# Optimization experiments

Measured on AMD Instinct MI355X. Metric: run time of the kernel, lower is better.

## Reference

```python
import jax, jax.numpy as jnp
import numpy as np

B_IN, B_L1, B_L2 = 64, 16, 8
F1, F2, F_OUT = 64, 128, 10
BATCH = 16
CPLX = jnp.complex64

# ---------- numpy precompute: quadrature weights, Wigner-d matrices, grids ----------

def _dh_weights(b):
    # Driscoll-Healy quadrature weights over the 2b beta samples
    j = np.arange(2 * b)
    l = np.arange(b)
    s = np.sin(np.outer(2 * j + 1, 2 * l + 1) * np.pi / (4 * b)) @ (1.0 / (2 * l + 1))
    return ((2.0 / b) * np.sin(np.pi * (2 * j + 1) / (4 * b)) * s).astype(np.float32)

def _wigner_d_all(lmax, betas):
    # d^l(beta) = exp(-i beta Jy) via eigendecomposition of Jy (quantum convention)
    betas = np.asarray(betas, np.float64)
    out = []
    for l in range(lmax + 1):
        m = np.arange(-l, l)
        cp = np.sqrt(l * (l + 1) - m * (m + 1))
        Jy = np.zeros((2 * l + 1, 2 * l + 1), np.complex128)
        Jy[np.arange(1, 2 * l + 1), np.arange(0, 2 * l)] = -0.5j * cp
        Jy[np.arange(0, 2 * l), np.arange(1, 2 * l + 1)] = 0.5j * cp
        lam, V = np.linalg.eigh(Jy)
        ph = np.exp(-1j * np.outer(betas, lam))
        d = np.einsum('mk,bk,nk->bmn', V, ph, V.conj())
        out.append(np.ascontiguousarray(d.real.astype(np.float32)))
    return out

def _s2_grid():
    beta = np.arange(1, 4) * (np.pi / 8) / 3
    alpha = np.linspace(0, 2 * np.pi, 8, endpoint=False)
    B, A = np.meshgrid(beta, alpha, indexing='ij')
    return B.ravel(), A.ravel()

def _so3_grid():
    beta = np.arange(1, 4) * (np.pi / 8) / 3
    alpha = np.linspace(0, 2 * np.pi, 8, endpoint=False)
    pre_gamma = np.linspace(0, 2 * np.pi, 8, endpoint=False)
    B, A, C = np.meshgrid(beta, alpha, pre_gamma, indexing='ij')
    return B.ravel(), A.ravel(), (C - A).ravel()

_BETAS_IN = np.pi * (2 * np.arange(2 * B_IN) + 1) / (4 * B_IN)
_BETAS_L1 = np.pi * (2 * np.arange(2 * B_L1) + 1) / (4 * B_L1)
_BETAS_L2 = np.pi * (2 * np.arange(2 * B_L2) + 1) / (4 * B_L2)
_W_IN = jnp.asarray(_dh_weights(B_IN))
_W_L1 = jnp.asarray(_dh_weights(B_L1))
_W_L2 = jnp.asarray(_dh_weights(B_L2))
_D_IN = _wigner_d_all(B_L1 - 1, _BETAS_IN)
_D_L1 = _wigner_d_all(B_L1 - 1, _BETAS_L1)
_D_L2 = _wigner_d_all(B_L2 - 1, _BETAS_L2)
_GB2, _GA2 = _s2_grid()
_GB3, _GA3, _GC3 = _so3_grid()
_D_G2 = _wigner_d_all(B_L1 - 1, _GB2)
_D_G3 = _wigner_d_all(B_L2 - 1, _GB3)

# spherical-harmonic / Wigner-D basis evaluated at kernel grid points
_PSI_S2 = []
for l in range(B_L1):
    m = np.arange(-l, l + 1)
    _PSI_S2.append(jnp.asarray((_D_G2[l][:, :, l].T * np.exp(-1j * np.outer(m, _GA2))).astype(np.complex64)))
_PSI_SO3 = []
for l in range(B_L2):
    m = np.arange(-l, l + 1)
    em = np.exp(-1j * np.outer(m, _GA3))
    en = np.exp(-1j * np.outer(m, _GC3))
    _PSI_SO3.append(jnp.asarray((_D_G3[l].transpose(1, 2, 0) * em[:, None, :] * en[None, :, :]).astype(np.complex64)))
_DCOL_IN = [jnp.asarray(_D_IN[l][:, :, l]) for l in range(B_L1)]  # d^l_{m,0}(beta_k)
_D_L1_J = [jnp.asarray(d) for d in _D_L1]
_D_L2_J = [jnp.asarray(d) for d in _D_L2]

# ---------- jax forward ----------

def _s2_fft(x):
    # x: [batch, f, 2b_in, 2b_in] (beta, alpha) -> list over l of [2l+1, batch, f] complex
    n = 2 * B_IN
    xf = jnp.fft.fft(x.astype(CPLX), axis=-1)  # e^{-i m alpha}
    out = []
    for l in range(B_L1):
        mi = np.arange(-l, l + 1) % n
        Xl = xf[..., mi]  # [batch, f, 2b, 2l+1]
        out.append(jnp.einsum('k,km,bfkm->mbf', _W_IN, _DCOL_IN[l], Xl) * (2 * np.pi / n))
    return out

def _so3_ifft(Fz, d_list, b):
    # Fz: list over l of [2l+1, 2l+1, batch, f] -> real [batch, f, 2b, 2b, 2b] (beta,alpha,gamma)
    n = 2 * b
    batch, f = Fz[0].shape[2], Fz[0].shape[3]
    S = jnp.zeros((batch, f, n, n, n), CPLX)
    for l in range(b):
        mi = np.arange(-l, l + 1) % n
        C = (2 * l + 1) * jnp.einsum('kmn,mnbf->bfkmn', d_list[l].astype(CPLX), Fz[l])
        S = S.at[:, :, :, mi[:, None], mi[None, :]].add(C)
    return jnp.real(jnp.fft.ifft2(S, axes=(-2, -1))) * (n * n)  # e^{+i m alpha} e^{+i n gamma}

def _so3_fft(x, d_list, w, b_l):
    # x: [batch, f, 2b, 2b, 2b] real -> list over l<b_l of [2l+1, 2l+1, batch, f] complex
    n = x.shape[-1]
    xf = jnp.fft.fft2(x.astype(CPLX), axes=(-2, -1)) / (n * n)
    out = []
    for l in range(b_l):
        mi = np.arange(-l, l + 1) % n
        Xl = xf[:, :, :, mi[:, None], mi[None, :]]  # [batch, f, 2b, 2l+1, 2l+1]
        out.append(jnp.einsum('k,kmn,bfkmn->mnbf', w, d_list[l], Xl) * (2 * np.pi))
    return out

def _forward(x, w1, w2, lin_w, lin_b):
    # S2Convolution: spectral x spectral-kernel outer product per degree l
    Fx = _s2_fft(x)
    Fy = [jnp.einsum('iog,mg->mio', w1.astype(CPLX), p) for p in _PSI_S2]
    Fz = [jnp.einsum('mbi,nio->mnbo', Fx[l], jnp.conj(Fy[l])) for l in range(B_L1)]
    y1 = jax.nn.relu(_so3_ifft(Fz, _D_L1_J, B_L1))
    # SO3Convolution
    Fx2 = _so3_fft(y1, _D_L1_J, _W_L1, B_L2)
    Fy2 = [jnp.einsum('iog,mng->mnio', w2.astype(CPLX), p) for p in _PSI_SO3]
    Fz2 = [jnp.einsum('mkbi,nkio->mnbo', Fx2[l], jnp.conj(Fy2[l])) for l in range(B_L2)]
    y2 = jax.nn.relu(_so3_ifft(Fz2, _D_L2_J, B_L2))
    # so3_integrate: quadrature over beta, uniform mean over alpha,gamma
    feat = jnp.einsum('k,bfk->bf', _W_L2, y2.mean(axis=(-2, -1)))
    return feat @ lin_w.T + lin_b


def setup_inputs() -> dict:
    key = jax.random.key(0)
    k1, k2, k3, k4 = jax.random.split(key, 4)
    x = jax.random.normal(k1, (BATCH, 1, 2 * B_IN, 2 * B_IN), jnp.float32)
    w1 = jax.random.normal(k2, (1, F1, 24), jnp.float32) / np.float32(np.sqrt(24))
    w2 = jax.random.normal(k3, (F1, F2, 192), jnp.float32) / np.float32(np.sqrt(192 * F1))
    lin_w = jax.random.normal(k4, (F_OUT, F2), jnp.float32) / np.float32(np.sqrt(F2))
    lin_b = jnp.zeros((F_OUT,), jnp.float32)
    return {'x': x, 'w1': w1, 'w2': w2, 'lin_w': lin_w, 'lin_b': lin_b}


def reference(x, w1, w2, lin_w, lin_b):
    return _forward(x, w1, w2, lin_w, lin_b)
```

## Files before the change

### kernel.cpp

```cpp
#include <hip/hip_runtime.h>
#include <cmath>
#include <vector>
#include <algorithm>

enum : int {
  OFF_WIN  = 0,
  OFF_WL1  = 128,
  OFF_WL2  = 160,
  OFF_DCOL = 176,
  OFF_D1A  = OFF_DCOL + 32768,
  OFF_D1B  = OFF_D1A + 174592,
  OFF_D2   = OFF_D1B + 174592,
  OFF_PSI2 = OFF_D2 + 10880,
  OFF_PSI3 = OFF_PSI2 + 12288,
  CONST_TOTAL = OFF_PSI3 + 261120
};

static constexpr size_t OFS_XF1  = 0;
static constexpr size_t OFS_FX   = 507904;
static constexpr size_t OFS_FY1  = 540672;
static constexpr size_t OFS_FX2  = 671744;
static constexpr size_t OFS_FY2  = 6242304;
static constexpr size_t OFS_FZ2  = 50806784;
static constexpr size_t OFS_W2T  = OFS_FZ2;
static constexpr size_t OFS_FEAT = 61947904;
static constexpr size_t WS_NEEDED = 61956096;

static inline int off3h(int l){ return (4*l*l*l - l)/3; }

namespace {

double fact_[32];
void init_fact(){ fact_[0]=1.0; for(int i=1;i<32;i++) fact_[i]=fact_[i-1]*i; }

void wigner_d(int l, double beta, double* d){
  int n = 2*l+1;
  double cb = std::cos(beta*0.5), sb = std::sin(beta*0.5);
  for(int r=0;r<n;r++){ int mp = r-l;
    for(int c=0;c<n;c++){ int m = c-l;
      double f = std::sqrt(fact_[l+mp]*fact_[l-mp]*fact_[l+m]*fact_[l-m]);
      int s0 = std::max(0, m-mp), s1 = std::min(l+m, l-mp);
      double sum = 0;
      for(int s=s0;s<=s1;s++){
        double t = (((mp-m+s)&1)? -1.0 : 1.0)
                 / (fact_[l+m-s]*fact_[s]*fact_[mp-m+s]*fact_[l-mp-s]);
        t *= std::pow(cb, (double)(2*l+m-mp-2*s)) * std::pow(sb, (double)(mp-m+2*s));
        sum += t;
      }
      d[r*n+c] = f*sum;
    }
  }
}

void dh_weights(int b, double* w){
  for(int j=0;j<2*b;j++){
    double s = 0;
    for(int l=0;l<b;l++) s += std::sin((2.0*j+1)*(2.0*l+1)*M_PI/(4.0*b))/(2.0*l+1);
    w[j] = (2.0/b)*std::sin(M_PI*(2.0*j+1)/(4.0*b))*s;
  }
}

float* g_const = nullptr;

struct ConstInit {
  ConstInit(){
    init_fact();
    std::vector<float> h((size_t)CONST_TOTAL, 0.0f);
    std::vector<double> tmp(31*31);
    std::vector<double> wl1(32);
    { std::vector<double> w(128); dh_weights(64, w.data()); for(int i=0;i<128;i++) h[OFF_WIN+i]=(float)w[i]; }
    { dh_weights(16, wl1.data()); for(int i=0;i<32;i++)  h[OFF_WL1+i]=(float)wl1[i]; }
    { std::vector<double> w(16);  dh_weights(8,  w.data()); for(int i=0;i<16;i++)  h[OFF_WL2+i]=(float)w[i]; }
    for(int l=0;l<16;l++){ int n=2*l+1;
      for(int k=0;k<128;k++){
        wigner_d(l, M_PI*(2.0*k+1)/256.0, tmp.data());
        for(int mi=0;mi<n;mi++) h[OFF_DCOL + (size_t)(l*l+mi)*128 + k] = (float)tmp[mi*n + l];
      }
    }
    for(int l=0;l<16;l++){ int n=2*l+1;
      for(int k=0;k<32;k++){
        wigner_d(l, M_PI*(2.0*k+1)/64.0, tmp.data());
        for(int t=0;t<n*n;t++){
          size_t base = (size_t)(off3h(l)+t)*32 + k;
          h[OFF_D1A + base] = (float)((2*l+1)*tmp[t]);
          if(l < 8)
            h[OFF_D1B + base] = (float)(2.0*M_PI*wl1[k]*tmp[t]/1024.0);
        }
      }
    }
    for(int l=0;l<8;l++){ int n=2*l+1;
      for(int k=0;k<16;k++){
        wigner_d(l, M_PI*(2.0*k+1)/32.0, tmp.data());
        for(int t=0;t<n*n;t++)
          h[OFF_D2 + (size_t)(off3h(l)+t)*16 + k] = (float)((2*l+1)*tmp[t]);
      }
    }
    for(int l=0;l<16;l++){ int n=2*l+1;
      for(int i=0;i<3;i++){
        wigner_d(l, (i+1)*(M_PI/8.0)/3.0, tmp.data());
        for(int j=0;j<8;j++){
          double alpha = 2.0*M_PI*j/8.0;
          int g = i*8+j;
          for(int mi=0;mi<n;mi++){
            double d = tmp[mi*n + l];
            double th = (double)(mi-l)*alpha;
            size_t base = OFF_PSI2 + ((size_t)(l*l+mi)*24 + g)*2;
            h[base+0] = (float)( d*std::cos(th));
            h[base+1] = (float)(-d*std::sin(th));
          }
        }
      }
    }
    for(int l=0;l<8;l++){ int n=2*l+1;
      for(int i=0;i<3;i++){
        wigner_d(l, (i+1)*(M_PI/8.0)/3.0, tmp.data());
        for(int j=0;j<8;j++){
          double alpha = 2.0*M_PI*j/8.0;
          for(int kk=0;kk<8;kk++){
            double gamma = 2.0*M_PI*kk/8.0 - alpha;
            int g = (i*8+j)*8+kk;
            for(int mi=0;mi<n;mi++) for(int ni=0;ni<n;ni++){
              double d = tmp[mi*n+ni];
              double th = (double)(mi-l)*alpha + (double)(ni-l)*gamma;
              size_t base = OFF_PSI3 + (((size_t)off3h(l)+ (size_t)mi*n+ni)*192 + g)*2;
              h[base+0] = (float)( d*std::cos(th));
              h[base+1] = (float)(-d*std::sin(th));
            }
          }
        }
      }
    }
    hipMalloc((void**)&g_const, sizeof(float)*(size_t)CONST_TOTAL);
    hipMemcpy(g_const, h.data(), sizeof(float)*(size_t)CONST_TOTAL, hipMemcpyHostToDevice);
  }
};
ConstInit g_init_;

}

__device__ __forceinline__ int off3d(int l){ return (4*l*l*l - l)/3; }
constexpr float TWO_PI_F = 6.28318530717958647692f;

__device__ __forceinline__ unsigned int f2bf(float f){
  union { float f; unsigned int u; } v; v.f = f;
  unsigned int r = v.u + 0x7FFFu + ((v.u >> 16) & 1u);
  return r >> 16;
}
__device__ __forceinline__ unsigned int pk2(float2 v){
  return f2bf(v.x) | (f2bf(v.y) << 16);
}
__device__ __forceinline__ float bflo(unsigned int u){
  union { unsigned int u; float f; } c; c.u = u << 16; return c.f;
}
__device__ __forceinline__ float bfhi(unsigned int u){
  union { unsigned int u; float f; } c; c.u = u & 0xffff0000u; return c.f;
}

typedef __attribute__((ext_vector_type(8))) short bf16x8;
typedef __attribute__((ext_vector_type(4))) float f32x4;

__global__ void k_fft_alpha(const float* __restrict__ x, float2* __restrict__ xf1){
  __shared__ float row[128];
  __shared__ float2 w128[128];
  __shared__ float2 red2[4][31];
  int r = blockIdx.x;
  int t = threadIdx.x;
  row[t] = x[(size_t)r*128 + t];
  float ang = (TWO_PI_F/128.0f)*t;
  w128[t] = make_float2(cosf(ang), sinf(ang));
  __syncthreads();
  int mi = t & 31, part = t >> 5;
  if(mi < 31){
    int m = mi - 15;
    float2 acc = make_float2(0.f,0.f);
    int a0 = part*32;
    for(int a=a0;a<a0+32;a++){
      float2 w = w128[(m*a)&127];
      acc.x += row[a]*w.x;
      acc.y -= row[a]*w.y;
    }
    red2[part][mi] = acc;
  }
  __syncthreads();
  if(t < 31){
    float2 s = red2[0][t];
    float2 s1 = red2[1][t], s2 = red2[2][t], s3 = red2[3][t];
    s.x += s1.x + s2.x + s3.x;
    s.y += s1.y + s2.y + s3.y;
    xf1[(size_t)r*31 + t] = s;
  }
}

__global__ void k_fx(const float* __restrict__ cst, const float2* __restrict__ xf1,
                     float2* __restrict__ FxP){
  __shared__ float2 redL[256];
  int lp = threadIdx.x & 63;
  int kc = threadIdx.x >> 6;
  int idx = blockIdx.x*64 + lp;
  int c2 = idx >> 4, b = idx & 15;
  int l = 0; while((l+1)*(l+1) <= c2) l++;
  int m = (c2 - l*l) - l;
  const float* W  = cst + OFF_WIN;
  const float* DC = cst + OFF_DCOL + (size_t)c2*128;
  float2 acc = make_float2(0.f,0.f);
  int k0 = kc*32;
  for(int k=k0;k<k0+32;k++){
    float wv = W[k]*DC[k];
    float2 xv = xf1[((size_t)b*128+k)*31 + (m+15)];
    acc.x += wv*xv.x; acc.y += wv*xv.y;
  }
  redL[threadIdx.x] = acc;
  __syncthreads();
  if(kc == 0){
    float2 p1 = redL[lp+64], p2 = redL[lp+128], p3 = redL[lp+192];
    acc.x += p1.x + p2.x + p3.x;
    acc.y += p1.y + p2.y + p3.y;
    float s = TWO_PI_F/128.0f;
    FxP[(size_t)c2*16+b] = make_float2(acc.x*s, acc.y*s);
  }
}

__global__ void k_fy1(const float* __restrict__ cst, const float* __restrict__ w1,
                      float2* __restrict__ FyP){
  int idx = blockIdx.x*blockDim.x + threadIdx.x;
  int c2 = idx >> 6, o = idx & 63;
  const float2* psi = (const float2*)(cst + OFF_PSI2) + (size_t)c2*24;
  const float* w1r = w1 + (size_t)o*24;
  float2 acc = make_float2(0.f,0.f);
  for(int g=0;g<24;g++){
    float wv = w1r[g];
    float2 p = psi[g];
    acc.x += wv*p.x; acc.y += wv*p.y;
  }
  FyP[(size_t)c2*64+o] = acc;
}

__global__ void __launch_bounds__(256,4) k_conv1(const float* __restrict__ cst,
                                                 const float2* __restrict__ FxP,
                                                 const float2* __restrict__ FyP,
                                                 unsigned int* __restrict__ FxB){
  __shared__ __align__(16) char L[39936];
  float2* FxL = (float2*)L;
  float2* FyL = FxL + 256;
  float2* SB  = (float2*)(L + 4096);
  unsigned int* yBu = (unsigned int*)(L + 4096);
  float2* XfB = (float2*)(L + 4096);
  unsigned int* TBu = (unsigned int*)(L + 23936);
  float2* T2B = (float2*)(L + 23936);
  float2* acc2= (float2*)(L + 34176);
  float2* w32 = (float2*)(L + 39616);
  int*    o3T = (int*)(L + 39872);

  int b = blockIdx.x >> 6, o = blockIdx.x & 63;
  int tid = threadIdx.x;
  if(tid < 32){ float ang = (TWO_PI_F/32.0f)*tid; w32[tid] = make_float2(cosf(ang), sinf(ang)); }
  if(tid < 16){ int l = tid; o3T[l] = (4*l*l*l - l)/3; }
  FxL[tid] = FxP[(size_t)tid*16 + b];
  FyL[tid] = FyP[(size_t)tid*64 + o];
  for(int t=tid; t<680; t+=256) acc2[t] = make_float2(0.f,0.f);

  const float* D1A = cst + OFF_D1A;
  const float* D1B = cst + OFF_D1B;

  for(int kt=0; kt<8; kt++){
    int k0 = kt*4;
    __syncthreads();
    for(int t=tid; t<496; t+=256){
      int mi = t/31, niq = t - mi*31;
      int n = niq-15;
      int an = n<0?-n:n;
      int lmin = mi>an?mi:an;
      float2 s0={0,0},s1={0,0},s2={0,0},s3={0,0};
      for(int l=lmin;l<16;l++){
        int c = 2*l+1, l2 = l*l;
        float2 fx = FxL[l2+l+mi];
        float2 fy = FyL[l2+(n+l)];
        float zx = fx.x*fy.x + fx.y*fy.y;
        float zy = fx.y*fy.x - fx.x*fy.y;
        const float4* dp = (const float4*)(D1A + (((size_t)o3T[l] + (mi+l)*c + (n+l))<<5) + k0);
        float4 d0 = dp[0];
        s0.x += d0.x*zx; s0.y += d0.x*zy;
        s1.x += d0.y*zx; s1.y += d0.y*zy;
        s2.x += d0.z*zx; s2.y += d0.z*zy;
        s3.x += d0.w*zx; s3.y += d0.w*zy;
      }
      float2* sp = SB + (size_t)t*5;
      sp[0]=s0; sp[1]=s1; sp[2]=s2; sp[3]=s3;
    }
    __syncthreads();
    {
      int mi = tid >> 4, cp = tid & 15;
      float2 a0[4], a1[4];
      #pragma unroll
      for(int j=0;j<4;j++){ a0[j]=make_float2(0,0); a1[j]=make_float2(0,0); }
      float2 step = w32[cp];
      float2 wv = w32[(15*cp)&31];
      float2 cur = make_float2(wv.x, -wv.y);
      const float2* srow = SB + (size_t)(mi*31)*5;
      for(int nb=0; nb<31; nb++){
        float2 q0 = srow[nb*5+0], q1 = srow[nb*5+1], q2 = srow[nb*5+2], q3 = srow[nb*5+3];
        float px, py;
        bool odd = (nb & 1);
        #define K1STEP(QX,QY,J) \
          px = QX*cur.x - QY*cur.y; py = QX*cur.y + QY*cur.x; \
          a0[J].x += px; a0[J].y += py; \
          if(odd){ a1[J].x += px; a1[J].y += py; } else { a1[J].x -= px; a1[J].y -= py; }
        K1STEP(q0.x,q0.y,0) K1STEP(q1.x,q1.y,1)
        K1STEP(q2.x,q2.y,2) K1STEP(q3.x,q3.y,3)
        #undef K1STEP
        float nx = cur.x*step.x - cur.y*step.y;
        cur.y = cur.x*step.y + cur.y*step.x;
        cur.x = nx;
      }
      unsigned int* tp0 = TBu + (size_t)(mi*32+cp)*5;
      tp0[0]=pk2(a0[0]); tp0[1]=pk2(a0[1]); tp0[2]=pk2(a0[2]); tp0[3]=pk2(a0[3]);
      unsigned int* tp1 = TBu + (size_t)(mi*32+cp+16)*5;
      tp1[0]=pk2(a1[0]); tp1[1]=pk2(a1[1]); tp1[2]=pk2(a1[2]); tp1[3]=pk2(a1[3]);
    }
    __syncthreads();
    {
      int c = tid & 31, aq = tid >> 5;
      float y0[4],y1[4],y2[4],y3[4], t0x[4];
      {
        const unsigned int* t0p = TBu + (size_t)c*5;
        t0x[0]=bflo(t0p[0]); t0x[1]=bflo(t0p[1]); t0x[2]=bflo(t0p[2]); t0x[3]=bflo(t0p[3]);
      }
      #pragma unroll
      for(int j=0;j<4;j++){ y0[j]=0; y1[j]=0; y2[j]=0; y3[j]=0; }
      #pragma unroll
      for(int m=1;m<16;m++){
        float2 w = w32[(m*aq)&31];
        const unsigned int* tp = TBu + (size_t)(m*32+c)*5;
        unsigned int d0=tp[0], d1=tp[1], d2=tp[2], d3=tp[3];
        float tx[4] = {bflo(d0),bflo(d1),bflo(d2),bflo(d3)};
        float ty[4] = {bfhi(d0),bfhi(d1),bfhi(d2),bfhi(d3)};
        #pragma unroll
        for(int j=0;j<4;j++){
          float px = tx[j]*w.x - ty[j]*w.y;
          float py = tx[j]*w.y + ty[j]*w.x;
          y0[j] += px;
          int r = m & 3;
          if(r==0){ y1[j] += px; y3[j] += px; }
          else if(r==1){ y1[j] -= py; y3[j] += py; }
          else if(r==2){ y1[j] -= px; y3[j] -= px; }
          else { y1[j] += py; y3[j] -= py; }
          y2[j] += (m&1)? -px : px;
        }
      }
      #define YWRITE(A, YV) { \
        float v0 = t0x[0]+2.f*YV[0], v1 = t0x[1]+2.f*YV[1], v2 = t0x[2]+2.f*YV[2], v3 = t0x[3]+2.f*YV[3]; \
        v0 = v0>0?v0:0; v1 = v1>0?v1:0; v2 = v2>0?v2:0; v3 = v3>0?v3:0; \
        unsigned int* yp = yBu + ((size_t)(A)*32 + c)*3; \
        yp[0] = f2bf(v0) | (f2bf(v1)<<16); \
        yp[1] = f2bf(v2) | (f2bf(v3)<<16); }
      YWRITE(aq,    y0)
      YWRITE(aq+8,  y1)
      YWRITE(aq+16, y2)
      YWRITE(aq+24, y3)
      #undef YWRITE
    }
    __syncthreads();
    {
      int mp = tid >> 5, c4 = tid & 31;
      float2 t2[4];
      #pragma unroll
      for(int j=0;j<4;j++) t2[j]=make_float2(0,0);
      for(int a=0;a<32;a++){
        float2 w = w32[(mp*a)&31];
        const unsigned int* yp = yBu + ((size_t)a*32 + c4)*3;
        unsigned int d0 = yp[0], d1 = yp[1];
        float yv[4] = {bflo(d0), bfhi(d0), bflo(d1), bfhi(d1)};
        #pragma unroll
        for(int j=0;j<4;j++){
          t2[j].x += yv[j]*w.x;
          t2[j].y -= yv[j]*w.y;
        }
      }
      float2* tp = T2B + (size_t)(mp*32+c4)*5;
      tp[0]=t2[0]; tp[1]=t2[1]; tp[2]=t2[2]; tp[3]=t2[3];
    }
    __syncthreads();
    if(tid < 120){
      int mp = tid/15, npq = tid - mp*15;
      int np = npq-7;
      float2 xf[4];
      #pragma unroll
      for(int j=0;j<4;j++) xf[j]=make_float2(0,0);
      float2 wv = w32[np&31];
      float2 step = make_float2(wv.x, -wv.y);
      float2 cur = make_float2(1.f, 0.f);
      const float2* trow = T2B + (size_t)(mp*32)*5;
      for(int c=0;c<32;c++){
        float2 q0 = trow[c*5+0], q1 = trow[c*5+1], q2 = trow[c*5+2], q3 = trow[c*5+3];
        float tx[4] = {q0.x,q1.x,q2.x,q3.x};
        float ty[4] = {q0.y,q1.y,q2.y,q3.y};
        #pragma unroll
        for(int j=0;j<4;j++){
          xf[j].x += tx[j]*cur.x - ty[j]*cur.y;
          xf[j].y += tx[j]*cur.y + ty[j]*cur.x;
        }
        float nx = cur.x*step.x - cur.y*step.y;
        cur.y = cur.x*step.y + cur.y*step.x;
        cur.x = nx;
      }
      float2* xp = XfB + (size_t)tid*5;
      xp[0]=xf[0]; xp[1]=xf[1]; xp[2]=xf[2]; xp[3]=xf[3];
    }
    __syncthreads();
    if(tid < 225){
      int mi2 = tid/15, ni2 = tid - mi2*15;
      int mp = mi2-7, np = ni2-7;
      float2 xf[4];
      if(mp >= 0){
        const float2* xp = XfB + (size_t)(mp*15+ni2)*5;
        xf[0]=xp[0]; xf[1]=xp[1]; xf[2]=xp[2]; xf[3]=xp[3];
      } else {
        const float2* xp = XfB + (size_t)((-mp)*15+(14-ni2))*5;
        float2 q0=xp[0],q1=xp[1],q2=xp[2],q3=xp[3];
        xf[0]=make_float2(q0.x,-q0.y); xf[1]=make_float2(q1.x,-q1.y);
        xf[2]=make_float2(q2.x,-q2.y); xf[3]=make_float2(q3.x,-q3.y);
      }
      int am = mp<0?-mp:mp, an = np<0?-np:np;
      int lmin = am>an?am:an;
      for(int l=lmin;l<8;l++){
        int c2 = 2*l+1;
        int cidx = o3T[l] + (mp+l)*c2 + (np+l);
        const float4* dp = (const float4*)(D1B + (((size_t)cidx)<<5) + k0);
        float4 d0 = dp[0];
        float rx = d0.x*xf[0].x + d0.y*xf[1].x + d0.z*xf[2].x + d0.w*xf[3].x;
        float ry = d0.x*xf[0].y + d0.y*xf[1].y + d0.z*xf[2].y + d0.w*xf[3].y;
        float2 cur = acc2[cidx];
        cur.x += rx; cur.y += ry;
        acc2[cidx] = cur;
      }
    }
  }
  __syncthreads();
  for(int t=tid; t<680; t+=256){
    float2 v = acc2[t];
    unsigned int pk = f2bf(v.x) | (f2bf(v.y) << 16);
    FxB[(size_t)t*1024 + b*64 + o] = pk;
  }
}

__global__ void k_w2t(const float* __restrict__ w2, float* __restrict__ w2t){
  int idx = blockIdx.x*256 + threadIdx.x;
  int g = idx >> 13, q = idx & 8191;
  int i = q & 63, o = q >> 6;
  w2t[idx] = w2[((size_t)i*128 + o)*192 + g];
}

__global__ void __launch_bounds__(256) k_fy2(const float* __restrict__ cst,
                                             const float* __restrict__ w2t,
                                             unsigned int* __restrict__ FyB){
  __shared__ __align__(16) float2 psiL[8*192];
  int cg  = blockIdx.x >> 5;
  int iog = blockIdx.x & 31;
  int tid = threadIdx.x;
  int q   = iog*256 + tid;
  int i   = q & 63, o = q >> 6;
  const float2* psi = (const float2*)(cst + OFF_PSI3) + (size_t)cg*8*192;
  for(int t=tid; t<1536; t+=256) psiL[t] = psi[t];
  __syncthreads();
  float2 acc[8];
  #pragma unroll
  for(int j=0;j<8;j++) acc[j] = make_float2(0.f,0.f);
  const float4* psiL4 = (const float4*)psiL;
  for(int g=0; g<192; g+=2){
    float w0 = w2t[(size_t)g*8192 + q];
    float w1 = w2t[(size_t)(g+1)*8192 + q];
    int gh = g >> 1;
    #pragma unroll
    for(int j=0;j<8;j++){
      float4 p = psiL4[j*96 + gh];
      acc[j].x += w0*p.x + w1*p.z;
      acc[j].y += w0*p.y + w1*p.w;
    }
  }
  #pragma unroll
  for(int j=0;j<8;j++){
    size_t base = (size_t)(cg*8+j)*16384;
    unsigned int r  = f2bf(acc[j].x);
    unsigned int im = f2bf(acc[j].y);
    unsigned int nim= f2bf(-acc[j].y);
    FyB[base + (size_t)(2*o  )*64 + i] = r  | (im << 16);
    FyB[base + (size_t)(2*o+1)*64 + i] = nim| (r  << 16);
  }
}

__global__ void __launch_bounds__(256) k_fz2(const unsigned int* __restrict__ FxB,
                                             const unsigned int* __restrict__ FyB,
                                             float* __restrict__ Fz2f){
  int p = blockIdx.x;
  int c, o3, q;
  if(p < 225)      { c=15; o3=455; q=p; }
  else if(p < 394) { c=13; o3=286; q=p-225; }
  else if(p < 515) { c=11; o3=165; q=p-394; }
  else if(p < 596) { c=9;  o3=84;  q=p-515; }
  else if(p < 645) { c=7;  o3=35;  q=p-596; }
  else if(p < 670) { c=5;  o3=10;  q=p-645; }
  else if(p < 679) { c=3;  o3=1;   q=p-670; }
  else             { c=1;  o3=0;   q=0; }
  int mi = q / c, ni = q - mi*c;

  int tid  = threadIdx.x;
  int lane = tid & 63, wv = tid >> 6;
  int m16  = lane & 15, quad = lane >> 4;

  int aoff = m16*128 + quad*8;
  int boff = (wv*64 + m16)*128 + quad*8;

  f32x4 acc0 = {0,0,0,0}, acc1 = {0,0,0,0}, acc2v = {0,0,0,0}, acc3 = {0,0,0,0};

  const unsigned short* FxS = (const unsigned short*)FxB;
  const unsigned short* FyS = (const unsigned short*)FyB;

  for(int kk=0; kk<c; kk++){
    const unsigned short* Arow = FxS + (size_t)(o3 + mi*c + kk)*2048;
    const unsigned short* Brow = FyS + (size_t)(o3 + ni*c + kk)*32768;
    #pragma unroll
    for(int ig=0; ig<4; ig++){
      bf16x8 af = *(const bf16x8*)(Arow + aoff + ig*32);
      bf16x8 b0 = *(const bf16x8*)(Brow + boff            + ig*32);
      bf16x8 b1 = *(const bf16x8*)(Brow + boff + 1*2048   + ig*32);
      bf16x8 b2 = *(const bf16x8*)(Brow + boff + 2*2048   + ig*32);
      bf16x8 b3 = *(const bf16x8*)(Brow + boff + 3*2048   + ig*32);
      acc0  = __builtin_amdgcn_mfma_f32_16x16x32_bf16(af, b0, acc0,  0,0,0);
      acc1  = __builtin_amdgcn_mfma_f32_16x16x32_bf16(af, b1, acc1,  0,0,0);
      acc2v = __builtin_amdgcn_mfma_f32_16x16x32_bf16(af, b2, acc2v, 0,0,0);
      acc3  = __builtin_amdgcn_mfma_f32_16x16x32_bf16(af, b3, acc3,  0,0,0);
    }
  }
  int coefC = o3 + mi*c + ni;
  float* dst = Fz2f + (size_t)coefC*4096;
  int npb = wv*64 + m16;
  #pragma unroll
  for(int r=0;r<4;r++){
    int b = quad*4 + r;
    dst[(size_t)b*256 + npb       ] = acc0[r];
    dst[(size_t)b*256 + npb + 16  ] = acc1[r];
    dst[(size_t)b*256 + npb + 32  ] = acc2v[r];
    dst[(size_t)b*256 + npb + 48  ] = acc3[r];
  }
}

__global__ void __launch_bounds__(256) k_slice2(const float* __restrict__ cst,
                                                const float2* __restrict__ Fz2P,
                                                float* __restrict__ featP){
  __shared__ float2 FzL[680];
  __shared__ float2 S2[225];
  __shared__ float2 TA[240];
  __shared__ float2 w16[16];
  __shared__ float red[256];
  int bo = blockIdx.x;
  int tid = threadIdx.x;
  if(tid < 16){ float ang = (TWO_PI_F/16.0f)*tid; w16[tid] = make_float2(cosf(ang), sinf(ang)); }
  for(int t=tid; t<680; t+=256) FzL[t] = Fz2P[(size_t)t*2048 + bo];
  __syncthreads();
  const float* D2  = cst + OFF_D2;
  const float* WL2 = cst + OFF_WL2;
  float part = 0.f;
  for(int k2=0;k2<16;k2++){
    if(tid < 225){
      int mi = tid/15, ni = tid%15;
      int m = mi-7, n = ni-7;
      int am = m<0?-m:m, an = n<0?-n:n;
      int lmin = am>an?am:an;
      float2 acc = make_float2(0.f,0.f);
      for(int l=lmin;l<8;l++){
        int c = 2*l+1;
        int idx = off3d(l) + (m+l)*c + (n+l);
        float dv = D2[((size_t)idx<<4) + k2];
        float2 fzv = FzL[idx];
        acc.x += dv*fzv.x; acc.y += dv*fzv.y;
      }
      S2[tid] = acc;
    }
    __syncthreads();
    if(tid < 240){
      int mi = tid >> 4, c = tid & 15;
      float2 acc = make_float2(0.f,0.f);
      for(int ni=0;ni<15;ni++){
        float2 sv = S2[mi*15+ni];
        float2 w = w16[((ni-7)*c)&15];
        acc.x += sv.x*w.x - sv.y*w.y;
        acc.y += sv.x*w.y + sv.y*w.x;
      }
      TA[mi*16+c] = acc;
    }
    __syncthreads();
    {
      int a = tid >> 4, c = tid & 15;
      float acc = 0.f;
      for(int mi=0;mi<15;mi++){
        float2 tv = TA[mi*16+c];
        float2 w = w16[((mi-7)*a)&15];
        acc += tv.x*w.x - tv.y*w.y;
      }
      if(acc > 0.f) part += WL2[k2]*acc;
    }
    __syncthreads();
  }
  red[tid] = part;
  __syncthreads();
  for(int s=128;s>0;s>>=1){ if(tid<s) red[tid]+=red[tid+s]; __syncthreads(); }
  if(tid==0) featP[bo] = red[0]*(1.0f/256.0f);
}

__global__ void k_out(const float* __restrict__ featP, const float* __restrict__ lin_w,
                      const float* __restrict__ lin_b, float* __restrict__ out){
  int t = threadIdx.x;
  if(t < 160){
    int b = t/10, j = t%10;
    float acc = lin_b[j];
    for(int o=0;o<128;o++) acc += featP[b*128+o]*lin_w[j*128+o];
    out[t] = acc;
  }
}

extern "C" void kernel_launch(void* const* d_in, const int* in_sizes, int n_in,
                              void* d_out, int out_size, void* d_ws, size_t ws_size,
                              hipStream_t stream){
  const float* x     = (const float*)d_in[0];
  const float* w1    = (const float*)d_in[1];
  const float* w2    = (const float*)d_in[2];
  const float* lin_w = (const float*)d_in[3];
  const float* lin_b = (const float*)d_in[4];
  float* out = (float*)d_out;
  if(ws_size < WS_NEEDED) return;
  char* ws = (char*)d_ws;
  float2* xf1  = (float2*)(ws + OFS_XF1);
  float2* FxP  = (float2*)(ws + OFS_FX);
  float2* FyP  = (float2*)(ws + OFS_FY1);
  unsigned int* FxB = (unsigned int*)(ws + OFS_FX2);
  unsigned int* FyB = (unsigned int*)(ws + OFS_FY2);
  float2* Fz2P = (float2*)(ws + OFS_FZ2);
  float*  w2tP = (float*)(ws + OFS_W2T);
  float*  featP= (float*)(ws + OFS_FEAT);
  const float* cst = g_const;

  k_fft_alpha<<<2048, 128, 0, stream>>>(x, xf1);
  k_fx      <<<64,   256, 0, stream>>>(cst, xf1, FxP);
  k_fy1     <<<64,   256, 0, stream>>>(cst, w1, FyP);
  k_conv1   <<<1024, 256, 0, stream>>>(cst, FxP, FyP, FxB);
  k_w2t     <<<6144, 256, 0, stream>>>(w2, w2tP);
  k_fy2     <<<2720, 256, 0, stream>>>(cst, w2tP, FyB);
  k_fz2     <<<680,  256, 0, stream>>>(FxB, FyB, (float*)Fz2P);
  k_slice2  <<<2048, 256, 0, stream>>>(cst, Fz2P, featP);
  k_out     <<<1,    256, 0, stream>>>(featP, lin_w, lin_b, out);
}
```

Measured before the change: 618.9 us.

## Exploit Wigner-D conjugate symmetry in conv1 and fz2; wave-per-item slice2

In conv1, the separate stage that expands half-plane Fourier coefficients to the full m range is fused into the alpha-DFT stage. Each thread now accumulates both the (m,n) and mirrored (-m,-n) Wigner terms using the conjugate symmetry, which removes one shared-memory round trip and one barrier. In fz2, only half of the (m,n) coefficient blocks are computed and the mirrored ones are written with a sign, roughly halving the blocks launched. slice2 now gives each wavefront its own batch/feature item, uses wave-level fences and a shuffle reduction instead of block barriers, and launches a quarter as many blocks. The cost is more shared memory per block and reliance on the exact symmetry sign conventions.

```diff
diff --git a/kernel.cpp b/kernel.cpp
--- a/kernel.cpp
+++ b/kernel.cpp
@@ -154,6 +154,11 @@
 }
 __device__ __forceinline__ float bfhi(unsigned int u){
   union { unsigned int u; float f; } c; c.u = u & 0xffff0000u; return c.f;
+}
+__device__ __forceinline__ void wave_fence(){
+  __asm__ volatile("" ::: "memory");
+  __builtin_amdgcn_s_waitcnt(0);
+  __asm__ volatile("" ::: "memory");
 }
 
 typedef __attribute__((ext_vector_type(8))) short bf16x8;
@@ -244,7 +249,6 @@
   float2* FyL = FxL + 256;
   float2* SB  = (float2*)(L + 4096);
   unsigned int* yBu = (unsigned int*)(L + 4096);
-  float2* XfB = (float2*)(L + 4096);
   unsigned int* TBu = (unsigned int*)(L + 23936);
   float2* T2B = (float2*)(L + 23936);
   float2* acc2= (float2*)(L + 34176);
@@ -383,55 +387,43 @@
     if(tid < 120){
       int mp = tid/15, npq = tid - mp*15;
       int np = npq-7;
-      float2 xf[4];
-      #pragma unroll
-      for(int j=0;j<4;j++) xf[j]=make_float2(0,0);
+      float2 xf0={0,0}, xf1v={0,0}, xf2={0,0}, xf3={0,0};
       float2 wv = w32[np&31];
       float2 step = make_float2(wv.x, -wv.y);
       float2 cur = make_float2(1.f, 0.f);
       const float2* trow = T2B + (size_t)(mp*32)*5;
       for(int c=0;c<32;c++){
         float2 q0 = trow[c*5+0], q1 = trow[c*5+1], q2 = trow[c*5+2], q3 = trow[c*5+3];
-        float tx[4] = {q0.x,q1.x,q2.x,q3.x};
-        float ty[4] = {q0.y,q1.y,q2.y,q3.y};
-        #pragma unroll
-        for(int j=0;j<4;j++){
-          xf[j].x += tx[j]*cur.x - ty[j]*cur.y;
-          xf[j].y += tx[j]*cur.y + ty[j]*cur.x;
-        }
+        xf0.x  += q0.x*cur.x - q0.y*cur.y;  xf0.y  += q0.x*cur.y + q0.y*cur.x;
+        xf1v.x += q1.x*cur.x - q1.y*cur.y;  xf1v.y += q1.x*cur.y + q1.y*cur.x;
+        xf2.x  += q2.x*cur.x - q2.y*cur.y;  xf2.y  += q2.x*cur.y + q2.y*cur.x;
+        xf3.x  += q3.x*cur.x - q3.y*cur.y;  xf3.y  += q3.x*cur.y + q3.y*cur.x;
         float nx = cur.x*step.x - cur.y*step.y;
         cur.y = cur.x*step.y + cur.y*step.x;
         cur.x = nx;
       }
-      float2* xp = XfB + (size_t)tid*5;
-      xp[0]=xf[0]; xp[1]=xf[1]; xp[2]=xf[2]; xp[3]=xf[3];
-    }
-    __syncthreads();
-    if(tid < 225){
-      int mi2 = tid/15, ni2 = tid - mi2*15;
-      int mp = mi2-7, np = ni2-7;
-      float2 xf[4];
-      if(mp >= 0){
-        const float2* xp = XfB + (size_t)(mp*15+ni2)*5;
-        xf[0]=xp[0]; xf[1]=xp[1]; xf[2]=xp[2]; xf[3]=xp[3];
-      } else {
-        const float2* xp = XfB + (size_t)((-mp)*15+(14-ni2))*5;
-        float2 q0=xp[0],q1=xp[1],q2=xp[2],q3=xp[3];
-        xf[0]=make_float2(q0.x,-q0.y); xf[1]=make_float2(q1.x,-q1.y);
-        xf[2]=make_float2(q2.x,-q2.y); xf[3]=make_float2(q3.x,-q3.y);
-      }
-      int am = mp<0?-mp:mp, an = np<0?-np:np;
-      int lmin = am>an?am:an;
+      int an = np<0?-np:np;
+      int lmin = mp>an?mp:an;
       for(int l=lmin;l<8;l++){
         int c2 = 2*l+1;
         int cidx = o3T[l] + (mp+l)*c2 + (np+l);
         const float4* dp = (const float4*)(D1B + (((size_t)cidx)<<5) + k0);
         float4 d0 = dp[0];
-        float rx = d0.x*xf[0].x + d0.y*xf[1].x + d0.z*xf[2].x + d0.w*xf[3].x;
-        float ry = d0.x*xf[0].y + d0.y*xf[1].y + d0.z*xf[2].y + d0.w*xf[3].y;
-        float2 cur = acc2[cidx];
-        cur.x += rx; cur.y += ry;
-        acc2[cidx] = cur;
+        float rx = d0.x*xf0.x + d0.y*xf1v.x + d0.z*xf2.x + d0.w*xf3.x;
+        float ry = d0.x*xf0.y + d0.y*xf1v.y + d0.z*xf2.y + d0.w*xf3.y;
+        float2 cu = acc2[cidx];
+        cu.x += rx; cu.y += ry;
+        acc2[cidx] = cu;
+        if(mp > 0){
+          int cidx2 = o3T[l] + (l-mp)*c2 + (l-np);
+          const float4* dp2 = (const float4*)(D1B + (((size_t)cidx2)<<5) + k0);
+          float4 d2 = dp2[0];
+          float rx2 = d2.x*xf0.x + d2.y*xf1v.x + d2.z*xf2.x + d2.w*xf3.x;
+          float ry2 = -(d2.x*xf0.y + d2.y*xf1v.y + d2.z*xf2.y + d2.w*xf3.y);
+          float2 cu2 = acc2[cidx2];
+          cu2.x += rx2; cu2.y += ry2;
+          acc2[cidx2] = cu2;
+        }
       }
     }
   }
@@ -493,15 +485,16 @@
                                              float* __restrict__ Fz2f){
   int p = blockIdx.x;
   int c, o3, q;
-  if(p < 225)      { c=15; o3=455; q=p; }
-  else if(p < 394) { c=13; o3=286; q=p-225; }
-  else if(p < 515) { c=11; o3=165; q=p-394; }
-  else if(p < 596) { c=9;  o3=84;  q=p-515; }
-  else if(p < 645) { c=7;  o3=35;  q=p-596; }
-  else if(p < 670) { c=5;  o3=10;  q=p-645; }
-  else if(p < 679) { c=3;  o3=1;   q=p-670; }
+  if(p < 113)      { c=15; o3=455; q=p; }
+  else if(p < 198) { c=13; o3=286; q=p-113; }
+  else if(p < 259) { c=11; o3=165; q=p-198; }
+  else if(p < 300) { c=9;  o3=84;  q=p-259; }
+  else if(p < 325) { c=7;  o3=35;  q=p-300; }
+  else if(p < 338) { c=5;  o3=10;  q=p-325; }
+  else if(p < 343) { c=3;  o3=1;   q=p-338; }
   else             { c=1;  o3=0;   q=0; }
   int mi = q / c, ni = q - mi*c;
+  int lh = c >> 1;
 
   int tid  = threadIdx.x;
   int lane = tid & 63, wv = tid >> 6;
@@ -542,27 +535,43 @@
     dst[(size_t)b*256 + npb + 32  ] = acc2v[r];
     dst[(size_t)b*256 + npb + 48  ] = acc3[r];
   }
-}
-
-__global__ void __launch_bounds__(256) k_slice2(const float* __restrict__ cst,
-                                                const float2* __restrict__ Fz2P,
-                                                float* __restrict__ featP){
-  __shared__ float2 FzL[680];
-  __shared__ float2 S2[225];
-  __shared__ float2 TA[240];
-  __shared__ float2 w16[16];
-  __shared__ float red[256];
-  int bo = blockIdx.x;
+  if(!(mi==lh && ni==lh)){
+    int coefM = o3 + (c-1-mi)*c + (c-1-ni);
+    float sg = (((mi+ni) + (m16&1)) & 1) ? -1.f : 1.f;
+    float* dst2 = Fz2f + (size_t)coefM*4096;
+    #pragma unroll
+    for(int r=0;r<4;r++){
+      int b = quad*4 + r;
+      dst2[(size_t)b*256 + npb       ] = sg*acc0[r];
+      dst2[(size_t)b*256 + npb + 16  ] = sg*acc1[r];
+      dst2[(size_t)b*256 + npb + 32  ] = sg*acc2v[r];
+      dst2[(size_t)b*256 + npb + 48  ] = sg*acc3[r];
+    }
+  }
+}
+
+__global__ void __launch_bounds__(256,4) k_slice2(const float* __restrict__ cst,
+                                                  const float2* __restrict__ Fz2P,
+                                                  float* __restrict__ featP){
+  __shared__ float2 FzL[4][680];
+  __shared__ float2 S2m[4][225];
+  __shared__ float2 TAm[4][240];
+  __shared__ float2 w16s[16];
   int tid = threadIdx.x;
-  if(tid < 16){ float ang = (TWO_PI_F/16.0f)*tid; w16[tid] = make_float2(cosf(ang), sinf(ang)); }
-  for(int t=tid; t<680; t+=256) FzL[t] = Fz2P[(size_t)t*2048 + bo];
+  int wvi = tid >> 6, lane = tid & 63;
+  int bo = blockIdx.x*4 + wvi;
+  if(tid < 16){ float ang = (TWO_PI_F/16.0f)*tid; w16s[tid] = make_float2(cosf(ang), sinf(ang)); }
+  float2* Fz = FzL[wvi];
+  float2* S  = S2m[wvi];
+  float2* T  = TAm[wvi];
+  for(int t=lane; t<680; t+=64) Fz[t] = Fz2P[(size_t)t*2048 + bo];
   __syncthreads();
   const float* D2  = cst + OFF_D2;
   const float* WL2 = cst + OFF_WL2;
   float part = 0.f;
   for(int k2=0;k2<16;k2++){
-    if(tid < 225){
-      int mi = tid/15, ni = tid%15;
+    for(int e=lane; e<225; e+=64){
+      int mi = e/15, ni = e - mi*15;
       int m = mi-7, n = ni-7;
       int am = m<0?-m:m, an = n<0?-n:n;
       int lmin = am>an?am:an;
@@ -571,40 +580,38 @@
         int c = 2*l+1;
         int idx = off3d(l) + (m+l)*c + (n+l);
         float dv = D2[((size_t)idx<<4) + k2];
-        float2 fzv = FzL[idx];
+        float2 fzv = Fz[idx];
         acc.x += dv*fzv.x; acc.y += dv*fzv.y;
       }
-      S2[tid] = acc;
-    }
-    __syncthreads();
-    if(tid < 240){
-      int mi = tid >> 4, c = tid & 15;
+      S[e] = acc;
+    }
+    wave_fence();
+    for(int e=lane; e<240; e+=64){
+      int mi = e >> 4, cc = e & 15;
       float2 acc = make_float2(0.f,0.f);
       for(int ni=0;ni<15;ni++){
-        float2 sv = S2[mi*15+ni];
-        float2 w = w16[((ni-7)*c)&15];
+        float2 sv = S[mi*15+ni];
+        float2 w = w16s[((ni-7)*cc)&15];
         acc.x += sv.x*w.x - sv.y*w.y;
         acc.y += sv.x*w.y + sv.y*w.x;
       }
-      TA[mi*16+c] = acc;
-    }
-    __syncthreads();
-    {
-      int a = tid >> 4, c = tid & 15;
+      T[e] = acc;
+    }
+    wave_fence();
+    for(int e=lane; e<256; e+=64){
+      int a = e >> 4, cc = e & 15;
       float acc = 0.f;
       for(int mi=0;mi<15;mi++){
-        float2 tv = TA[mi*16+c];
-        float2 w = w16[((mi-7)*a)&15];
+        float2 tv = T[mi*16+cc];
+        float2 w = w16s[((mi-7)*a)&15];
         acc += tv.x*w.x - tv.y*w.y;
       }
       if(acc > 0.f) part += WL2[k2]*acc;
     }
-    __syncthreads();
-  }
-  red[tid] = part;
-  __syncthreads();
-  for(int s=128;s>0;s>>=1){ if(tid<s) red[tid]+=red[tid+s]; __syncthreads(); }
-  if(tid==0) featP[bo] = red[0]*(1.0f/256.0f);
+    wave_fence();
+  }
+  for(int s=32;s>0;s>>=1) part += __shfl_down(part, s, 64);
+  if(lane==0) featP[bo] = part*(1.0f/256.0f);
 }
 
 __global__ void k_out(const float* __restrict__ featP, const float* __restrict__ lin_w,
@@ -645,7 +652,7 @@
   k_conv1   <<<1024, 256, 0, stream>>>(cst, FxP, FyP, FxB);
   k_w2t     <<<6144, 256, 0, stream>>>(w2, w2tP);
   k_fy2     <<<2720, 256, 0, stream>>>(cst, w2tP, FyB);
-  k_fz2     <<<680,  256, 0, stream>>>(FxB, FyB, (float*)Fz2P);
-  k_slice2  <<<2048, 256, 0, stream>>>(cst, Fz2P, featP);
+  k_fz2     <<<344,  256, 0, stream>>>(FxB, FyB, (float*)Fz2P);
+  k_slice2  <<<512,  256, 0, stream>>>(cst, Fz2P, featP);
   k_out     <<<1,    256, 0, stream>>>(featP, lin_w, lin_b, out);
 }
```

Result: slower. 699.4 us (+13.0%).

## Exploit conjugate symmetry in Fz2 and split output columns across two blocks

Applied to the files above, without the earlier changes.

The Fz2 kernel now computes only about half of the (m,n) coefficient pairs per degree. The mirrored pair (c-1-m, c-1-n) is produced from the same accumulators with a parity-dependent sign, which relies on a symmetry of real-signal Wigner coefficients. Each pair is also split across two blocks by output-column half, so each wave holds two accumulators instead of four. This cuts MFMA work and B-operand loads roughly in half at the cost of a second store pass and correctness depending on the symmetry and sign rule.

```diff
diff --git a/kernel.cpp b/kernel.cpp
--- a/kernel.cpp
+++ b/kernel.cpp
@@ -491,26 +491,28 @@
 __global__ void __launch_bounds__(256) k_fz2(const unsigned int* __restrict__ FxB,
                                              const unsigned int* __restrict__ FyB,
                                              float* __restrict__ Fz2f){
-  int p = blockIdx.x;
+  int p = blockIdx.x >> 1, nb = blockIdx.x & 1;
   int c, o3, q;
-  if(p < 225)      { c=15; o3=455; q=p; }
-  else if(p < 394) { c=13; o3=286; q=p-225; }
-  else if(p < 515) { c=11; o3=165; q=p-394; }
-  else if(p < 596) { c=9;  o3=84;  q=p-515; }
-  else if(p < 645) { c=7;  o3=35;  q=p-596; }
-  else if(p < 670) { c=5;  o3=10;  q=p-645; }
-  else if(p < 679) { c=3;  o3=1;   q=p-670; }
+  if(p < 113)      { c=15; o3=455; q=p; }
+  else if(p < 198) { c=13; o3=286; q=p-113; }
+  else if(p < 259) { c=11; o3=165; q=p-198; }
+  else if(p < 300) { c=9;  o3=84;  q=p-259; }
+  else if(p < 325) { c=7;  o3=35;  q=p-300; }
+  else if(p < 338) { c=5;  o3=10;  q=p-325; }
+  else if(p < 343) { c=3;  o3=1;   q=p-338; }
   else             { c=1;  o3=0;   q=0; }
   int mi = q / c, ni = q - mi*c;
+  int lh = c >> 1;
 
   int tid  = threadIdx.x;
   int lane = tid & 63, wv = tid >> 6;
   int m16  = lane & 15, quad = lane >> 4;
 
+  int nrow = nb*128 + wv*32 + m16;
   int aoff = m16*128 + quad*8;
-  int boff = (wv*64 + m16)*128 + quad*8;
-
-  f32x4 acc0 = {0,0,0,0}, acc1 = {0,0,0,0}, acc2v = {0,0,0,0}, acc3 = {0,0,0,0};
+  int boff = nrow*128 + quad*8;
+
+  f32x4 acc0 = {0,0,0,0}, acc1 = {0,0,0,0};
 
   const unsigned short* FxS = (const unsigned short*)FxB;
   const unsigned short* FyS = (const unsigned short*)FyB;
@@ -521,26 +523,31 @@
     #pragma unroll
     for(int ig=0; ig<4; ig++){
       bf16x8 af = *(const bf16x8*)(Arow + aoff + ig*32);
-      bf16x8 b0 = *(const bf16x8*)(Brow + boff            + ig*32);
-      bf16x8 b1 = *(const bf16x8*)(Brow + boff + 1*2048   + ig*32);
-      bf16x8 b2 = *(const bf16x8*)(Brow + boff + 2*2048   + ig*32);
-      bf16x8 b3 = *(const bf16x8*)(Brow + boff + 3*2048   + ig*32);
-      acc0  = __builtin_amdgcn_mfma_f32_16x16x32_bf16(af, b0, acc0,  0,0,0);
-      acc1  = __builtin_amdgcn_mfma_f32_16x16x32_bf16(af, b1, acc1,  0,0,0);
-      acc2v = __builtin_amdgcn_mfma_f32_16x16x32_bf16(af, b2, acc2v, 0,0,0);
-      acc3  = __builtin_amdgcn_mfma_f32_16x16x32_bf16(af, b3, acc3,  0,0,0);
+      bf16x8 b0 = *(const bf16x8*)(Brow + boff          + ig*32);
+      bf16x8 b1 = *(const bf16x8*)(Brow + boff + 2048   + ig*32);
+      acc0 = __builtin_amdgcn_mfma_f32_16x16x32_bf16(af, b0, acc0, 0,0,0);
+      acc1 = __builtin_amdgcn_mfma_f32_16x16x32_bf16(af, b1, acc1, 0,0,0);
     }
   }
   int coefC = o3 + mi*c + ni;
   float* dst = Fz2f + (size_t)coefC*4096;
-  int npb = wv*64 + m16;
+  int npb = nrow;
   #pragma unroll
   for(int r=0;r<4;r++){
     int b = quad*4 + r;
-    dst[(size_t)b*256 + npb       ] = acc0[r];
-    dst[(size_t)b*256 + npb + 16  ] = acc1[r];
-    dst[(size_t)b*256 + npb + 32  ] = acc2v[r];
-    dst[(size_t)b*256 + npb + 48  ] = acc3[r];
+    dst[(size_t)b*256 + npb     ] = acc0[r];
+    dst[(size_t)b*256 + npb + 16] = acc1[r];
+  }
+  if(!(mi==lh && ni==lh)){
+    int coefM = o3 + (c-1-mi)*c + (c-1-ni);
+    float sg = (((mi+ni) + (npb&1)) & 1) ? -1.f : 1.f;
+    float* dst2 = Fz2f + (size_t)coefM*4096;
+    #pragma unroll
+    for(int r=0;r<4;r++){
+      int b = quad*4 + r;
+      dst2[(size_t)b*256 + npb     ] = sg*acc0[r];
+      dst2[(size_t)b*256 + npb + 16] = sg*acc1[r];
+    }
   }
 }
 
@@ -645,7 +652,7 @@
   k_conv1   <<<1024, 256, 0, stream>>>(cst, FxP, FyP, FxB);
   k_w2t     <<<6144, 256, 0, stream>>>(w2, w2tP);
   k_fy2     <<<2720, 256, 0, stream>>>(cst, w2tP, FyB);
-  k_fz2     <<<680,  256, 0, stream>>>(FxB, FyB, (float*)Fz2P);
+  k_fz2     <<<688,  256, 0, stream>>>(FxB, FyB, (float*)Fz2P);
   k_slice2  <<<2048, 256, 0, stream>>>(cst, Fz2P, featP);
   k_out     <<<1,    256, 0, stream>>>(featP, lin_w, lin_b, out);
 }
```

Result: faster. 598.1 us (-3.4%).
